# Performance work log

Measured on AMD Instinct MI355X. Metric: run time of the kernel, lower is better.

The kernel has to match this reference:

```python
import jax, jax.numpy as jnp
import numpy as np

B, S = 2, 1024
ENC_IN, MARK_IN = 21, 4
PRED_LEN, C_OUT = 96, 21
E = 512                 # embedding_dim
INNER = 2 * E           # proj_factor=2.0 (library default; Model does not pass it)
NH = 8                  # mLSTM heads
DH = INNER // NH        # 128
K = 4                   # causal conv1d kernel
BS = 4                  # qkv_proj_blocksize
NHP = INNER // BS       # 256 block-diagonal proj heads
NB = 4                  # num_blocks
EPS = 1e-5


def setup_inputs() -> dict:
    key = jax.random.key(0)
    ks = jax.random.split(key, 24)
    it = iter(range(24))
    def n(shape, s=0.02):
        return jax.random.normal(ks[next(it)], shape, jnp.float32) * s
    return {
        "x_enc": n((B, S, ENC_IN), 1.0),
        "x_mark_enc": n((B, S, MARK_IN), 1.0),
        "x_dec": n((B, PRED_LEN, ENC_IN), 1.0),
        "x_mark_dec": n((B, PRED_LEN, MARK_IN), 1.0),
        "emb_W": n((ENC_IN + MARK_IN, E), 0.05),
        "emb_b": jnp.zeros((E,), jnp.float32),
        "ln_w": jnp.ones((NB, E), jnp.float32),
        "up_W": n((NB, E, 2 * INNER)),
        "conv_W": n((NB, INNER, K), 0.1),
        "conv_b": jnp.zeros((NB, INNER), jnp.float32),
        "q_W": n((NB, NHP, BS, BS), 0.1),
        "k_W": n((NB, NHP, BS, BS), 0.1),
        "v_W": n((NB, NHP, BS, BS), 0.1),
        "ig_W": n((NB, 3 * INNER, NH)),
        "ig_b": jnp.zeros((NB, NH), jnp.float32),
        "fg_W": n((NB, 3 * INNER, NH)),
        "fg_b": jnp.tile(jnp.linspace(3.0, 6.0, NH, dtype=jnp.float32), (NB, 1)),
        "skip": jnp.ones((NB, INNER), jnp.float32),
        "onorm_w": jnp.ones((NB, INNER), jnp.float32),
        "down_W": n((NB, INNER, E)),
        "post_ln_w": jnp.ones((E,), jnp.float32),
        "head_W": n((E, C_OUT), 0.05),
        "head_b": jnp.zeros((C_OUT,), jnp.float32),
    }


def _ln(x, w):
    mu = jnp.mean(x, -1, keepdims=True)
    var = jnp.var(x, -1, keepdims=True)
    return (x - mu) * jax.lax.rsqrt(var + EPS) * w


def _headwise(x, w):
    # block-diagonal LinearHeadwiseExpand: (B,S,INNER) with (NHP,BS,BS) blocks
    xh = x.reshape(x.shape[0], x.shape[1], NHP, BS)
    return jnp.einsum('bshd,hod->bsho', xh, w).reshape(x.shape)


def _block(x, lw, uW, cW, cb, qW, kW, vW, igW, igb, fgW, fgb, sk, ow, dW):
    xn = _ln(x, lw)
    up = xn @ uW                                  # (B,S,2*INNER)
    xm, z = up[..., :INNER], up[..., INNER:]
    # causal depthwise conv1d + SiLU
    xc = jax.lax.conv_general_dilated(
        xm.transpose(0, 2, 1), cW[:, None, :], (1,), [(K - 1, 0)],
        feature_group_count=INNER,
        dimension_numbers=('NCH', 'OIH', 'NCH')).transpose(0, 2, 1) + cb
    xc = jax.nn.silu(xc)
    q = _headwise(xc, qW)
    k = _headwise(xc, kW)
    v = _headwise(xm, vW)
    qkv = jnp.concatenate([q, k, v], -1)          # (B,S,3*INNER)
    ig = (qkv @ igW + igb).transpose(0, 2, 1)     # (B,NH,S)
    fg = (qkv @ fgW + fgb).transpose(0, 2, 1)
    qh = q.reshape(B, S, NH, DH).transpose(0, 2, 1, 3)
    kh = k.reshape(B, S, NH, DH).transpose(0, 2, 1, 3)
    vh = v.reshape(B, S, NH, DH).transpose(0, 2, 1, 3)
    # parallel stabilized mLSTM (exp-gated linear attention)
    log_f = jax.nn.log_sigmoid(fg)
    cs = jnp.cumsum(log_f, -1)                    # (B,NH,S)
    Mmat = cs[..., :, None] - cs[..., None, :]    # (B,NH,S,S) cumulative decay
    tri = jnp.tril(jnp.ones((S, S), bool))
    logD = jnp.where(tri, Mmat + ig[..., None, :], -jnp.inf)
    m = jnp.max(logD, -1, keepdims=True)          # row-wise stabilizer
    D = jnp.exp(logD - m)
    qk = jnp.einsum('bnsd,bntd->bnst', qh, kh) / (DH ** 0.5)
    C = qk * D
    norm = jnp.maximum(jnp.abs(jnp.sum(C, -1, keepdims=True)), jnp.exp(-m))
    h = jnp.einsum('bnst,bntd->bnsd', C / (norm + 1e-6), vh)
    # multi-head layernorm (groupnorm over DH per head), weight, no bias
    hn = (h - jnp.mean(h, -1, keepdims=True)) * jax.lax.rsqrt(jnp.var(h, -1, keepdims=True) + EPS)
    hn = hn.transpose(0, 2, 1, 3).reshape(B, S, INNER) * ow
    hs = (hn + sk * xc) * jax.nn.silu(z)          # learnable skip + output gate
    return x + hs @ dW                            # residual


def reference(x_enc, x_mark_enc, x_dec, x_mark_dec, emb_W, emb_b, ln_w, up_W,
              conv_W, conv_b, q_W, k_W, v_W, ig_W, ig_b, fg_W, fg_b, skip,
              onorm_w, down_W, post_ln_w, head_W, head_b):
    x = jnp.concatenate([x_enc, x_mark_enc], -1) @ emb_W + emb_b
    for i in range(NB):
        x = _block(x, ln_w[i], up_W[i], conv_W[i], conv_b[i], q_W[i], k_W[i],
                   v_W[i], ig_W[i], ig_b[i], fg_W[i], fg_b[i], skip[i],
                   onorm_w[i], down_W[i])
    x = _ln(x, post_ln_w)
    return x[:, -PRED_LEN:, :] @ head_W + head_b
```

## Files before the change

### kernel.cpp

```cpp
#include <hip/hip_runtime.h>
#include <hip/hip_bf16.h>

#define S_LEN 1024
#define E_DIM 512
#define INNER_D 1024
#define NHEAD 8
#define DHEAD 128

typedef unsigned short u16;
typedef unsigned int u32;
typedef __attribute__((ext_vector_type(8))) short short8;
typedef __attribute__((ext_vector_type(4))) float f32x4;

union S8 { short8 v; u16 u[8]; uint4 q; };

__device__ __forceinline__ u16 f2bf(float f) {
  u32 u = __float_as_uint(f);
  u32 r = u + 0x7FFFu + ((u >> 16) & 1u);
  return (u16)(r >> 16);
}
__device__ __forceinline__ float bf2f(u16 u) { return __uint_as_float(((u32)u) << 16); }

__device__ __forceinline__ void gload16(const u16* g, u16* l) {
  __builtin_amdgcn_global_load_lds((const __attribute__((address_space(1))) void*)g,
                                   (__attribute__((address_space(3))) void*)l, 16, 0, 0);
}

__global__ __launch_bounds__(128) void embed_kernel(
    const float* __restrict__ xe, const float* __restrict__ xm,
    const float* __restrict__ W, const float* __restrict__ bias,
    float* __restrict__ x)
{
  int row = blockIdx.x;
  int tid = threadIdx.x;
  __shared__ float in_s[25];
  if (tid < 21) in_s[tid] = xe[row * 21 + tid];
  else if (tid < 25) in_s[tid] = xm[row * 4 + tid - 21];
  __syncthreads();
#pragma unroll
  for (int rep = 0; rep < 4; rep++) {
    int e = tid + rep * 128;
    float acc = bias[e];
#pragma unroll
    for (int i = 0; i < 25; i++) acc += in_s[i] * W[i * E_DIM + e];
    x[(size_t)row * E_DIM + e] = acc;
  }
}

__global__ __launch_bounds__(256) void ln_kernel(
    const float* __restrict__ x, const float* __restrict__ w, u16* __restrict__ out)
{
  int row = blockIdx.x, tid = threadIdx.x;
  const float* xr = x + (size_t)row * E_DIM;
  float2 v = *(const float2*)(xr + tid * 2);
  float s = v.x + v.y, q = v.x * v.x + v.y * v.y;
#pragma unroll
  for (int off = 32; off; off >>= 1) { s += __shfl_xor(s, off); q += __shfl_xor(q, off); }
  __shared__ float ssum[4], ssq[4];
  int wv = tid >> 6;
  if ((tid & 63) == 0) { ssum[wv] = s; ssq[wv] = q; }
  __syncthreads();
  s = ssum[0] + ssum[1] + ssum[2] + ssum[3];
  q = ssq[0] + ssq[1] + ssq[2] + ssq[3];
  float mu = s * (1.f / E_DIM);
  float var = q * (1.f / E_DIM) - mu * mu;
  float rs = rsqrtf(var + 1e-5f);
  int e = tid * 2;
  ushort2 o;
  o.x = f2bf((v.x - mu) * rs * w[e]);
  o.y = f2bf((v.y - mu) * rs * w[e + 1]);
  *(ushort2*)(out + (size_t)row * E_DIM + e) = o;
}

__global__ __launch_bounds__(256) void ln_final_kernel(
    const float* __restrict__ x, const float* __restrict__ w, float* __restrict__ out)
{
  int ridx = blockIdx.x;
  int b = ridx / 96, r = ridx % 96;
  int row = b * S_LEN + (S_LEN - 96) + r;
  int tid = threadIdx.x;
  const float* xr = x + (size_t)row * E_DIM;
  float2 v = *(const float2*)(xr + tid * 2);
  float s = v.x + v.y, q = v.x * v.x + v.y * v.y;
#pragma unroll
  for (int off = 32; off; off >>= 1) { s += __shfl_xor(s, off); q += __shfl_xor(q, off); }
  __shared__ float ssum[4], ssq[4];
  int wv = tid >> 6;
  if ((tid & 63) == 0) { ssum[wv] = s; ssq[wv] = q; }
  __syncthreads();
  s = ssum[0] + ssum[1] + ssum[2] + ssum[3];
  q = ssq[0] + ssq[1] + ssq[2] + ssq[3];
  float mu = s * (1.f / E_DIM);
  float var = q * (1.f / E_DIM) - mu * mu;
  float rs = rsqrtf(var + 1e-5f);
  int e = tid * 2;
  float2 o;
  o.x = (v.x - mu) * rs * w[e];
  o.y = (v.y - mu) * rs * w[e + 1];
  *(float2*)(out + (size_t)ridx * E_DIM + e) = o;
}

__global__ __launch_bounds__(256) void transpose_bf16_all_kernel(
    const float* __restrict__ in0, u16* __restrict__ out0, int K, int N)
{
  __shared__ u16 T[64][72];
  int L = blockIdx.z;
  const float* in = in0 + (size_t)L * K * N;
  u16* out = out0 + (size_t)L * N * K;
  int k0 = blockIdx.x * 64, n0 = blockIdx.y * 64;
  int t = threadIdx.x;
  int kr = t >> 2, nseg = (t & 3) * 16;
  const float* src = in + (size_t)(k0 + kr) * N + n0 + nseg;
#pragma unroll
  for (int j = 0; j < 16; j++) T[kr][nseg + j] = f2bf(src[j]);
  __syncthreads();
  int nr = t >> 2, kseg = (t & 3) * 16;
  u32 u[8];
#pragma unroll
  for (int rr = 0; rr < 8; rr++) {
    u32 lo = T[kseg + 2 * rr][nr];
    u32 hi = T[kseg + 2 * rr + 1][nr];
    u[rr] = lo | (hi << 16);
  }
  u16* dst = out + (size_t)(n0 + nr) * K + k0 + kseg;
  uint4 w0 = {u[0], u[1], u[2], u[3]};
  uint4 w1 = {u[4], u[5], u[6], u[7]};
  *(uint4*)dst = w0;
  *(uint4*)(dst + 8) = w1;
}

__global__ __launch_bounds__(256) void gates_w_transpose_kernel(
    const float* __restrict__ igW, const float* __restrict__ fgW,
    u16* __restrict__ hi, u16* __restrict__ lo)
{
  int L = blockIdx.z;
  int n = blockIdx.y;
  int k = blockIdx.x * 256 + threadIdx.x;
  const float* W = ((n < 8) ? igW : fgW) + (size_t)L * 24576;
  float v = W[(size_t)k * 8 + (n & 7)];
  u16 h = f2bf(v);
  u16 l = f2bf(v - bf2f(h));
  size_t o = ((size_t)L * 16 + n) * 3072 + k;
  hi[o] = h;
  lo[o] = l;
}

__global__ __launch_bounds__(256) void gemm_bf16_split64(
    const u16* __restrict__ A, const u16* __restrict__ Bt,
    float* __restrict__ C0, u16* __restrict__ C1,
    int M, int N, int K, int split_col, int ldc)
{
  __shared__ u16 As0[64 * 64], As1[64 * 64];
  __shared__ u16 Bs0[128 * 64], Bs1[128 * 64];
  const int tid = threadIdx.x;
  const int row0 = blockIdx.y * 64, col0 = blockIdx.x * 128;
  const int wave = tid >> 6, lane = tid & 63;
  const int wr = wave >> 1, wc = wave & 1;
  const int lm = lane & 15, lq = lane >> 4;
  const int lr = lane >> 3;
  const int cg = (lane & 7) ^ lr;
  f32x4 acc[2][4] = {};
  const u16* Abase = A + (size_t)(row0 + lr) * K + cg * 8;
  const u16* Bbase = Bt + (size_t)(col0 + lr) * K + cg * 8;
  const int key = lm & 7;

#define STAGE_UP(AS, BS, K0) do { \
  _Pragma("unroll") for (int i = 0; i < 2; i++) \
    gload16(Abase + (size_t)((wave * 2 + i) * 8) * K + (K0), &AS[(wave * 2 + i) * 512]); \
  _Pragma("unroll") for (int j = 0; j < 4; j++) \
    gload16(Bbase + (size_t)((wave * 4 + j) * 8) * K + (K0), &BS[(wave * 4 + j) * 512]); \
} while (0)

#define COMPUTE_UP(AS, BS) do { \
  short8 af[2][2], bfv[2][4]; \
  _Pragma("unroll") for (int kc = 0; kc < 2; kc++) { \
    _Pragma("unroll") for (int i = 0; i < 2; i++) \
      af[kc][i] = *(const short8*)&AS[(wr * 32 + i * 16 + lm) * 64 + (((kc * 4 + lq) ^ key) * 8)]; \
    _Pragma("unroll") for (int j = 0; j < 4; j++) \
      bfv[kc][j] = *(const short8*)&BS[(wc * 64 + j * 16 + lm) * 64 + (((kc * 4 + lq) ^ key) * 8)]; \
  } \
  _Pragma("unroll") for (int kc = 0; kc < 2; kc++) \
    _Pragma("unroll") for (int i = 0; i < 2; i++) \
      _Pragma("unroll") for (int j = 0; j < 4; j++) \
        acc[i][j] = __builtin_amdgcn_mfma_f32_16x16x32_bf16(af[kc][i], bfv[kc][j], acc[i][j], 0, 0, 0); \
} while (0)

  STAGE_UP(As0, Bs0, 0);
  STAGE_UP(As1, Bs1, 64);
#pragma unroll
  for (int t = 0; t < 8; t++) {
    if (t < 7) asm volatile("s_waitcnt vmcnt(6)" ::: "memory");
    else       asm volatile("s_waitcnt vmcnt(0)" ::: "memory");
    __builtin_amdgcn_sched_barrier(0);
    __builtin_amdgcn_s_barrier();
    if (t & 1) COMPUTE_UP(As1, Bs1); else COMPUTE_UP(As0, Bs0);
    __builtin_amdgcn_s_barrier();
    if (t + 2 < 8) {
      if (t & 1) STAGE_UP(As1, Bs1, (t + 2) * 64);
      else       STAGE_UP(As0, Bs0, (t + 2) * 64);
    }
  }
#undef STAGE_UP
#undef COMPUTE_UP

  const bool toC1 = (col0 >= split_col);
#pragma unroll
  for (int i = 0; i < 2; i++) {
#pragma unroll
    for (int j = 0; j < 4; j++) {
      int col = col0 - (toC1 ? split_col : 0) + wc * 64 + j * 16 + lm;
#pragma unroll
      for (int r = 0; r < 4; r++) {
        int row = row0 + wr * 32 + i * 16 + lq * 4 + r;
        if (toC1) C1[(size_t)row * ldc + col] = f2bf(acc[i][j][r]);
        else C0[(size_t)row * ldc + col] = acc[i][j][r];
      }
    }
  }
}

__global__ __launch_bounds__(256) void gemm_bf16_32(
    const u16* __restrict__ A, const u16* __restrict__ Bt,
    float* __restrict__ C, int M, int N, int K, int ldc)
{
  __shared__ u16 As0[64 * 64], As1[64 * 64];
  __shared__ u16 Bs0[64 * 64], Bs1[64 * 64];
  const int tid = threadIdx.x;
  const int row0 = blockIdx.y * 64, col0 = blockIdx.x * 64;
  const int wave = tid >> 6, lane = tid & 63;
  const int wr = wave >> 1, wc = wave & 1;
  const int lm = lane & 15, lq = lane >> 4;
  const int lr = lane >> 3;
  const int cg = (lane & 7) ^ lr;
  f32x4 acc[2][2] = {};
  const u16* Abase = A + (size_t)(row0 + lr) * K + cg * 8;
  const u16* Bbase = Bt + (size_t)(col0 + lr) * K + cg * 8;
  const int key = lm & 7;

#define STAGE_DN(AS, BS, K0) do { \
  _Pragma("unroll") for (int i = 0; i < 2; i++) \
    gload16(Abase + (size_t)((wave * 2 + i) * 8) * K + (K0), &AS[(wave * 2 + i) * 512]); \
  _Pragma("unroll") for (int j = 0; j < 2; j++) \
    gload16(Bbase + (size_t)((wave * 2 + j) * 8) * K + (K0), &BS[(wave * 2 + j) * 512]); \
} while (0)

#define COMPUTE_DN(AS, BS) do { \
  short8 af[2][2], bfv[2][2]; \
  _Pragma("unroll") for (int kc = 0; kc < 2; kc++) { \
    _Pragma("unroll") for (int i = 0; i < 2; i++) \
      af[kc][i] = *(const short8*)&AS[(wr * 32 + i * 16 + lm) * 64 + (((kc * 4 + lq) ^ key) * 8)]; \
    _Pragma("unroll") for (int j = 0; j < 2; j++) \
      bfv[kc][j] = *(const short8*)&BS[(wc * 32 + j * 16 + lm) * 64 + (((kc * 4 + lq) ^ key) * 8)]; \
  } \
  _Pragma("unroll") for (int kc = 0; kc < 2; kc++) \
    _Pragma("unroll") for (int i = 0; i < 2; i++) \
      _Pragma("unroll") for (int j = 0; j < 2; j++) \
        acc[i][j] = __builtin_amdgcn_mfma_f32_16x16x32_bf16(af[kc][i], bfv[kc][j], acc[i][j], 0, 0, 0); \
} while (0)

  STAGE_DN(As0, Bs0, 0);
  STAGE_DN(As1, Bs1, 64);
#pragma unroll
  for (int t = 0; t < 16; t++) {
    if (t < 15) asm volatile("s_waitcnt vmcnt(4)" ::: "memory");
    else        asm volatile("s_waitcnt vmcnt(0)" ::: "memory");
    __builtin_amdgcn_sched_barrier(0);
    __builtin_amdgcn_s_barrier();
    if (t & 1) COMPUTE_DN(As1, Bs1); else COMPUTE_DN(As0, Bs0);
    __builtin_amdgcn_s_barrier();
    if (t + 2 < 16) {
      if (t & 1) STAGE_DN(As1, Bs1, (t + 2) * 64);
      else       STAGE_DN(As0, Bs0, (t + 2) * 64);
    }
  }
#undef STAGE_DN
#undef COMPUTE_DN

#pragma unroll
  for (int i = 0; i < 2; i++) {
#pragma unroll
    for (int j = 0; j < 2; j++) {
      int col = col0 + wc * 32 + j * 16 + lm;
#pragma unroll
      for (int r = 0; r < 4; r++) {
        int row = row0 + wr * 32 + i * 16 + lq * 4 + r;
        C[(size_t)row * ldc + col] += acc[i][j][r];
      }
    }
  }
}

__global__ __launch_bounds__(256) void convqkv_kernel(
    const float* __restrict__ xm,
    const float* __restrict__ cw, const float* __restrict__ cb,
    const float* __restrict__ qw, const float* __restrict__ kw, const float* __restrict__ vw,
    float* __restrict__ xc, u16* __restrict__ q, u16* __restrict__ k, u16* __restrict__ v)
{
  int r0 = blockIdx.x * 4;
  int s0 = r0 & (S_LEN - 1);
  int g = threadIdx.x;
  int c0 = g * 4;
  const float* base = xm + (size_t)r0 * INNER_D + c0;

  float4 xv[7];
#pragma unroll
  for (int j = 0; j < 7; j++) {
    int ts = s0 - 3 + j;
    float4 t = {0.f, 0.f, 0.f, 0.f};
    if (ts >= 0) t = *(const float4*)(base + (ptrdiff_t)(j - 3) * INNER_D);
    xv[j] = t;
  }
  float cwv[4][4];
#pragma unroll
  for (int c = 0; c < 4; c++)
#pragma unroll
    for (int kk = 0; kk < 4; kk++) cwv[c][kk] = cw[(c0 + c) * 4 + kk];
  float cbv[4] = {cb[c0], cb[c0 + 1], cb[c0 + 2], cb[c0 + 3]};
  const float* qg = qw + g * 16;
  const float* kg = kw + g * 16;
  const float* vg = vw + g * 16;
  float qwv[16], kwv[16], vwv[16];
#pragma unroll
  for (int i = 0; i < 16; i++) { qwv[i] = qg[i]; kwv[i] = kg[i]; vwv[i] = vg[i]; }

#pragma unroll
  for (int i = 0; i < 4; i++) {
    float a0 = cbv[0], a1 = cbv[1], a2 = cbv[2], a3 = cbv[3];
#pragma unroll
    for (int kk = 0; kk < 4; kk++) {
      float4 xvv = xv[i + kk];
      a0 += xvv.x * cwv[0][kk];
      a1 += xvv.y * cwv[1][kk];
      a2 += xvv.z * cwv[2][kk];
      a3 += xvv.w * cwv[3][kk];
    }
    a0 = a0 / (1.f + __expf(-a0));
    a1 = a1 / (1.f + __expf(-a1));
    a2 = a2 / (1.f + __expf(-a2));
    a3 = a3 / (1.f + __expf(-a3));
    float4 accv = {a0, a1, a2, a3};
    *(float4*)(xc + (size_t)(r0 + i) * INNER_D + c0) = accv;

    float xcv[4] = {a0, a1, a2, a3};
    float xmv[4] = {xv[i + 3].x, xv[i + 3].y, xv[i + 3].z, xv[i + 3].w};
    ushort4 qs, ks, vs;
    u16* qp = (u16*)&qs; u16* kp = (u16*)&ks; u16* vp = (u16*)&vs;
#pragma unroll
    for (int o = 0; o < 4; o++) {
      float aq = 0.f, ak = 0.f, av = 0.f;
#pragma unroll
      for (int d = 0; d < 4; d++) {
        aq += xcv[d] * qwv[o * 4 + d];
        ak += xcv[d] * kwv[o * 4 + d];
        av += xmv[d] * vwv[o * 4 + d];
      }
      qp[o] = f2bf(aq); kp[o] = f2bf(ak); vp[o] = f2bf(av);
    }
    size_t off = (size_t)(r0 + i) * INNER_D + c0;
    *(ushort4*)(q + off) = qs;
    *(ushort4*)(k + off) = ks;
    *(ushort4*)(v + off) = vs;
  }
}

__global__ __launch_bounds__(256) void gates_mfma_kernel(
    const u16* __restrict__ q, const u16* __restrict__ k, const u16* __restrict__ v,
    const u16* __restrict__ whi, const u16* __restrict__ wlo,
    const float* __restrict__ igb, const float* __restrict__ fgb,
    float* __restrict__ ig, float* __restrict__ fg)
{
  const int blk = blockIdx.x;
  const int tid = threadIdx.x;
  const int wave = tid >> 6, lane = tid & 63;
  const int lm = lane & 15, lq = lane >> 4;
  const int grow = blk * 16 + lm;
  const u16* parts[3] = {q, k, v};
  f32x4 acc = {};
#pragma unroll 4
  for (int kc = 0; kc < 24; kc++) {
    int k0 = wave * 768 + kc * 32;
    int part = k0 >> 10;
    int idx = (k0 & 1023) + lq * 8;
    S8 a, bh_, bl_;
    a.q = *(const uint4*)(parts[part] + (size_t)grow * INNER_D + idx);
    bh_.q = *(const uint4*)(whi + (size_t)lm * 3072 + k0 + lq * 8);
    bl_.q = *(const uint4*)(wlo + (size_t)lm * 3072 + k0 + lq * 8);
    acc = __builtin_amdgcn_mfma_f32_16x16x32_bf16(a.v, bh_.v, acc, 0, 0, 0);
    acc = __builtin_amdgcn_mfma_f32_16x16x32_bf16(a.v, bl_.v, acc, 0, 0, 0);
  }
  __shared__ float red[4][16][17];
#pragma unroll
  for (int r = 0; r < 4; r++) red[wave][lq * 4 + r][lm] = acc[r];
  __syncthreads();
  if (wave == 0) {
#pragma unroll
    for (int r = 0; r < 4; r++) {
      int row = lq * 4 + r;
      float sum = red[0][row][lm] + red[1][row][lm] + red[2][row][lm] + red[3][row][lm];
      int growr = blk * 16 + row;
      int b = growr >> 10, s = growr & (S_LEN - 1);
      if (lm < 8) ig[((size_t)(b * NHEAD + lm) << 10) + s] = sum + igb[lm];
      else        fg[((size_t)(b * NHEAD + (lm - 8)) << 10) + s] = sum + fgb[lm - 8];
    }
  }
}

__global__ __launch_bounds__(1024) void scan_kernel(
    const float* __restrict__ ig, const float* __restrict__ fg,
    float* __restrict__ a, float* __restrict__ rm, float* __restrict__ enm)
{
  int bh = blockIdx.x;
  int t = threadIdx.x;
  int lane = t & 63, wv = t >> 6;
  __shared__ float sw[16];
  size_t o = ((size_t)bh << 10) + t;
  float f = fg[o];
  float lf = (f >= 0.f) ? -log1pf(__expf(-f)) : f - log1pf(__expf(f));
  float v = lf;
#pragma unroll
  for (int off = 1; off < 64; off <<= 1) {
    float u = __shfl_up(v, off);
    if (lane >= off) v += u;
  }
  if (lane == 63) sw[wv] = v;
  __syncthreads();
  float pre = 0.f;
  for (int w = 0; w < wv; w++) pre += sw[w];
  float cs = v + pre;
  float av = ig[o] - cs;
  a[o] = av;
  float m = av;
#pragma unroll
  for (int off = 1; off < 64; off <<= 1) {
    float u = __shfl_up(m, off);
    if (lane >= off) m = fmaxf(m, u);
  }
  __syncthreads();
  if (lane == 63) sw[wv] = m;
  __syncthreads();
  float pm = -3.4e38f;
  for (int w = 0; w < wv; w++) pm = fmaxf(pm, sw[w]);
  float rmx = fmaxf(m, pm);
  rm[o] = rmx;
  enm[o] = __expf(-(cs + rmx));
}

__device__ __constant__ int c_qt[24] = {7,15,14,15, 6,13,14,12,13, 5,11,12,10,11, 4, 9,10, 8, 9, 3, 8, 2, 1, 0};
__device__ __constant__ int c_k0[24] = {0, 0, 7, 8, 0, 0, 0, 6, 7, 0, 0, 0, 5, 6, 0, 0, 0, 4, 5, 0, 0, 0, 0, 0};
__device__ __constant__ int c_k1[24] = {8, 8,15,16, 7, 7, 7,13,14, 6, 6, 6,11,12, 5, 5, 5, 9,10, 4, 4, 3, 2, 1};
__device__ __constant__ int c_md[24] = {0, 1, 2, 2, 0, 1, 1, 2, 2, 0, 1, 1, 2, 2, 0, 1, 1, 2, 2, 0, 1, 0, 0, 0};

__global__ __launch_bounds__(256) void attn_mfma_kernel(
    const u16* __restrict__ qhg, const u16* __restrict__ khg, const u16* __restrict__ vhg,
    const float* __restrict__ a_arr, const float* __restrict__ rm_arr, const float* __restrict__ enm_arr,
    const float* __restrict__ xc, const u16* __restrict__ zh,
    const float* __restrict__ skip, const float* __restrict__ onw,
    u16* __restrict__ hs, float* __restrict__ hpart, float* __restrict__ scpart)
{
  const int bh = blockIdx.x;
  const int job = blockIdx.y;
  const int qt = c_qt[job], k0t = c_k0[job], k1t = c_k1[job], mode = c_md[job];
  const int b = bh >> 3, h = bh & 7;
  const int s0 = qt * 64;
  const int tid = threadIdx.x;
  const int wave = tid >> 6, lane = tid & 63;
  const int lm = lane & 15, lq = lane >> 4;
  const size_t rowbase = (size_t)b * S_LEN;
  const int c0 = h * DHEAD;

  __shared__ u16 Ks0[64 * 128], Ks1[64 * 128];
  __shared__ u16 Vt0[128 * 72], Vt1[128 * 72];
  __shared__ u16 Ws[64 * 72];
  __shared__ float as0[64], as1[64];

  short8 aq[4];
  {
    const u16* qp = qhg + (rowbase + s0 + wave * 16 + lm) * INNER_D + c0 + lq * 8;
#pragma unroll
    for (int kc = 0; kc < 4; kc++) {
      S8 tmp; tmp.q = *(const uint4*)(qp + kc * 32);
      aq[kc] = tmp.v;
    }
  }
  float rmv[4];
#pragma unroll
  for (int r = 0; r < 4; r++)
    rmv[r] = rm_arr[(size_t)bh * S_LEN + s0 + wave * 16 + lq * 4 + r];

  f32x4 accH[8] = {};
  float sc_acc[4] = {0.f, 0.f, 0.f, 0.f};
  const float scale = 0.08838834764831845f;
  const int lr16 = lane >> 4;
  const int ls16 = lane & 15;
  const int tp0 = tid & 31, dg0 = tid >> 5;
  const int dg1 = dg0 + 8;

  S8 vA0, vA1, vB0, vB1;
  float aval;

#define PREF_K(KS, T0) do { \
  _Pragma("unroll") for (int j = 0; j < 4; j++) { \
    int rK = (wave * 4 + j) * 4 + lr16; \
    int cgk = ls16 ^ (rK & 7); \
    gload16(khg + (rowbase + (T0) + rK) * INNER_D + c0 + cgk * 8, &KS[(wave * 4 + j) * 512]); \
  } \
} while (0)

#define PREF_V(T0) do { \
  const u16* sv = vhg + (rowbase + (T0) + 2 * tp0) * INNER_D + c0 + dg0 * 8; \
  vA0.q = *(const uint4*)sv; \
  vA1.q = *(const uint4*)(sv + INNER_D); \
  const u16* sw2 = vhg + (rowbase + (T0) + 2 * tp0) * INNER_D + c0 + dg1 * 8; \
  vB0.q = *(const uint4*)sw2; \
  vB1.q = *(const uint4*)(sw2 + INNER_D); \
  aval = (tid < 64) ? a_arr[(size_t)bh * S_LEN + (T0) + tid] : 0.f; \
} while (0)

#define WRITE_V(VT, ASB) do { \
  _Pragma("unroll") for (int j = 0; j < 8; j++) \
    *(u32*)&VT[(dg0 * 8 + j) * 72 + 2 * tp0] = (u32)vA0.u[j] | ((u32)vA1.u[j] << 16); \
  _Pragma("unroll") for (int j = 0; j < 8; j++) \
    *(u32*)&VT[(dg1 * 8 + j) * 72 + 2 * tp0] = (u32)vB0.u[j] | ((u32)vB1.u[j] << 16); \
  if (tid < 64) ASB[tid] = aval; \
} while (0)

#define QK_STEP(KS, PACC) do { \
  _Pragma("unroll") for (int kc = 0; kc < 4; kc++) \
    _Pragma("unroll") for (int cb = 0; cb < 4; cb++) { \
      short8 bk = *(const short8*)&KS[(cb * 16 + lm) * 128 + (((kc * 4 + lq) ^ (lm & 7)) * 8)]; \
      PACC[cb] = __builtin_amdgcn_mfma_f32_16x16x32_bf16(aq[kc], bk, PACC[cb], 0, 0, 0); \
    } \
} while (0)

#define W_PV(ASB, VT, T0, PACC) do { \
  float wpart[4] = {0.f, 0.f, 0.f, 0.f}; \
  _Pragma("unroll") for (int cb = 0; cb < 4; cb++) { \
    int colg = (T0) + cb * 16 + lm; \
    float ea = ASB[cb * 16 + lm]; \
    _Pragma("unroll") for (int r = 0; r < 4; r++) { \
      int rowg = s0 + wave * 16 + lq * 4 + r; \
      float wv = PACC[cb][r] * scale * __expf(ea - rmv[r]); \
      if (colg > rowg) wv = 0.f; \
      wpart[r] += wv; \
      Ws[(wave * 16 + lq * 4 + r) * 72 + cb * 16 + lm] = f2bf(wv); \
    } \
  } \
  _Pragma("unroll") for (int r = 0; r < 4; r++) { \
    float sr = wpart[r]; \
    sr += __shfl_xor(sr, 1); sr += __shfl_xor(sr, 2); \
    sr += __shfl_xor(sr, 4); sr += __shfl_xor(sr, 8); \
    sc_acc[r] += sr; \
  } \
  _Pragma("unroll") for (int kc = 0; kc < 2; kc++) { \
    short8 aw = *(const short8*)&Ws[(wave * 16 + lm) * 72 + kc * 32 + lq * 8]; \
    _Pragma("unroll") for (int nb = 0; nb < 8; nb++) { \
      short8 bv = *(const short8*)&VT[(nb * 16 + lm) * 72 + kc * 32 + lq * 8]; \
      accH[nb] = __builtin_amdgcn_mfma_f32_16x16x32_bf16(aw, bv, accH[nb], 0, 0, 0); \
    } \
  } \
} while (0)

  int kt = k0t;
  PREF_K(Ks0, kt * 64);
  PREF_V(kt * 64);
  WRITE_V(Vt0, as0);
  __syncthreads();

  while (true) {
    {
      bool more = (kt + 1 < k1t);
      if (more) { PREF_K(Ks1, (kt + 1) * 64); PREF_V((kt + 1) * 64); }
      f32x4 pacc[4] = {};
      QK_STEP(Ks0, pacc);
      if (more) WRITE_V(Vt1, as1);
      W_PV(as0, Vt0, kt * 64, pacc);
      __syncthreads();
      kt++;
      if (kt >= k1t) break;
    }
    {
      bool more = (kt + 1 < k1t);
      if (more) { PREF_K(Ks0, (kt + 1) * 64); PREF_V((kt + 1) * 64); }
      f32x4 pacc[4] = {};
      QK_STEP(Ks1, pacc);
      if (more) WRITE_V(Vt0, as0);
      W_PV(as1, Vt1, kt * 64, pacc);
      __syncthreads();
      kt++;
      if (kt >= k1t) break;
    }
  }
#undef PREF_K
#undef PREF_V
#undef WRITE_V
#undef QK_STEP
#undef W_PV

  if (mode != 0) {
    int slot = mode - 1;
    int qr = qt - 8;
    float* Hp = hpart + (((size_t)slot * 16 + bh) * 8 + qr) * 8192;
    float* sp = scpart + ((slot * 16 + bh) * 8 + qr) * 64;
#pragma unroll
    for (int r = 0; r < 4; r++) {
      int row = wave * 16 + lq * 4 + r;
      if (lm == 0) sp[row] = sc_acc[r];
#pragma unroll
      for (int nb = 0; nb < 8; nb++)
        Hp[row * 128 + nb * 16 + lm] = accH[nb][r];
    }
    return;
  }

  float inv[4], muv[4], rsv[4];
#pragma unroll
  for (int r = 0; r < 4; r++) {
    int rowg = s0 + wave * 16 + lq * 4 + r;
    float nrm = fmaxf(fabsf(sc_acc[r]), enm_arr[(size_t)bh * S_LEN + rowg]);
    inv[r] = 1.f / (nrm + 1e-6f);
  }
#pragma unroll
  for (int r = 0; r < 4; r++) {
    float s = 0.f, qq = 0.f;
#pragma unroll
    for (int nb = 0; nb < 8; nb++) {
      float hv = accH[nb][r] * inv[r];
      accH[nb][r] = hv;
      s += hv; qq += hv * hv;
    }
    s += __shfl_xor(s, 1); s += __shfl_xor(s, 2); s += __shfl_xor(s, 4); s += __shfl_xor(s, 8);
    qq += __shfl_xor(qq, 1); qq += __shfl_xor(qq, 2); qq += __shfl_xor(qq, 4); qq += __shfl_xor(qq, 8);
    float mu = s * (1.f / DHEAD);
    float var = qq * (1.f / DHEAD) - mu * mu;
    muv[r] = mu;
    rsv[r] = rsqrtf(var + 1e-5f);
  }
  float ow[8], sk[8];
#pragma unroll
  for (int nb = 0; nb < 8; nb++) {
    ow[nb] = onw[c0 + nb * 16 + lm];
    sk[nb] = skip[c0 + nb * 16 + lm];
  }
#pragma unroll
  for (int r = 0; r < 4; r++) {
    int rowg = s0 + wave * 16 + lq * 4 + r;
    size_t base = (rowbase + rowg) * INNER_D + c0;
#pragma unroll
    for (int nb = 0; nb < 8; nb++) {
      int d = nb * 16 + lm;
      float xcv = xc[base + d];
      float zv = bf2f(zh[base + d]);
      float hn = (accH[nb][r] - muv[r]) * rsv[r] * ow[nb] + sk[nb] * xcv;
      float o = hn * (zv / (1.f + __expf(-zv)));
      hs[base + d] = f2bf(o);
    }
  }
}

__global__ __launch_bounds__(256) void attn_combine_kernel(
    const float* __restrict__ hpart, const float* __restrict__ scpart,
    const float* __restrict__ enm,
    const float* __restrict__ xc, const u16* __restrict__ zh,
    const float* __restrict__ skip, const float* __restrict__ onw,
    u16* __restrict__ hs)
{
  int wave = threadIdx.x >> 6, lane = threadIdx.x & 63;
  int gid = blockIdx.x * 4 + wave;
  int bh = gid >> 9;
  int rr = gid & 511;
  int qr = rr >> 6, row = rr & 63;
  int b = bh >> 3, hh = bh & 7;
  int s = (qr + 8) * 64 + row;
  size_t off = (((size_t)bh) * 8 + qr) * 8192 + row * 128 + lane * 2;
  float2 h0 = *(const float2*)(hpart + off);
  float2 h1 = *(const float2*)(hpart + 1048576 + off);
  int sidx = (bh * 8 + qr) * 64 + row;
  float sc = scpart[sidx] + scpart[8192 + sidx];
  float nrm = fmaxf(fabsf(sc), enm[(size_t)bh * S_LEN + s]);
  float inv = 1.f / (nrm + 1e-6f);
  float hx = (h0.x + h1.x) * inv, hy = (h0.y + h1.y) * inv;
  float sm = hx + hy, sq = hx * hx + hy * hy;
#pragma unroll
  for (int off2 = 32; off2; off2 >>= 1) { sm += __shfl_xor(sm, off2); sq += __shfl_xor(sq, off2); }
  float mu = sm * (1.f / DHEAD);
  float var = sq * (1.f / DHEAD) - mu * mu;
  float rs = rsqrtf(var + 1e-5f);
  int c0 = hh * DHEAD + lane * 2;
  size_t base = ((size_t)(b * S_LEN + s)) * INNER_D + c0;
  float2 xc2 = *(const float2*)(xc + base);
  ushort2 z2u = *(const ushort2*)(zh + base);
  float z2x = bf2f(z2u.x), z2y = bf2f(z2u.y);
  float skx = skip[c0], sky = skip[c0 + 1];
  float owx = onw[c0],  owy = onw[c0 + 1];
  ushort2 o;
  o.x = f2bf(((hx - mu) * rs * owx + skx * xc2.x) * (z2x / (1.f + __expf(-z2x))));
  o.y = f2bf(((hy - mu) * rs * owy + sky * xc2.y) * (z2y / (1.f + __expf(-z2y))));
  *(ushort2*)(hs + base) = o;
}

__global__ __launch_bounds__(64) void head_kernel(
    const float* __restrict__ ln96, const float* __restrict__ hW, const float* __restrict__ hb,
    float* __restrict__ out)
{
  int row = blockIdx.x;
  int n = threadIdx.x;
  if (n >= 21) return;
  float acc = hb[n];
  const float* xr = ln96 + (size_t)row * E_DIM;
  for (int kk = 0; kk < E_DIM; kk++) acc += xr[kk] * hW[kk * 21 + n];
  out[row * 21 + n] = acc;
}

extern "C" void kernel_launch(void* const* d_in, const int* in_sizes, int n_in,
                              void* d_out, int out_size, void* d_ws, size_t ws_size,
                              hipStream_t stream)
{
  const float* x_enc   = (const float*)d_in[0];
  const float* x_mark  = (const float*)d_in[1];
  const float* emb_W   = (const float*)d_in[4];
  const float* emb_b   = (const float*)d_in[5];
  const float* ln_w    = (const float*)d_in[6];
  const float* up_W    = (const float*)d_in[7];
  const float* conv_W  = (const float*)d_in[8];
  const float* conv_b  = (const float*)d_in[9];
  const float* q_W     = (const float*)d_in[10];
  const float* k_W     = (const float*)d_in[11];
  const float* v_W     = (const float*)d_in[12];
  const float* ig_W    = (const float*)d_in[13];
  const float* ig_b    = (const float*)d_in[14];
  const float* fg_W    = (const float*)d_in[15];
  const float* fg_b    = (const float*)d_in[16];
  const float* skip_w  = (const float*)d_in[17];
  const float* onorm_w = (const float*)d_in[18];
  const float* down_W  = (const float*)d_in[19];
  const float* post_ln = (const float*)d_in[20];
  const float* head_W  = (const float*)d_in[21];
  const float* head_b  = (const float*)d_in[22];

  float* p = (float*)d_ws;
  float* x    = p; p += 1048576;
  float* xm   = p; p += 2097152;
  float* xc   = p; p += 2097152;
  float* igb_ = p; p += 16384;
  float* fgb_ = p; p += 16384;
  float* ab   = p; p += 16384;
  float* rmb  = p; p += 16384;
  float* enmb = p; p += 16384;
  float* ln96 = p; p += 98304;
  u16* qhb = (u16*)p; p += 1048576;
  u16* khb = (u16*)p; p += 1048576;
  u16* vhb = (u16*)p; p += 1048576;
  u16* zh  = (u16*)p; p += 524288;
  u16* xnh = (u16*)p; p += 524288;
  u16* upWtA = (u16*)p; p += 2097152;
  u16* dnWtA = (u16*)p; p += 1048576;
  u16* gtwH = (u16*)p; p += 98304;
  u16* gtwL = (u16*)p; p += 98304;
  float* hpart = p; p += 2097152;
  float* scpart = p; p += 16384;
  u16* hsbh = (u16*)xm;

  embed_kernel<<<2048, 128, 0, stream>>>(x_enc, x_mark, emb_W, emb_b, x);
  transpose_bf16_all_kernel<<<dim3(8, 32, 4), 256, 0, stream>>>(up_W, upWtA, 512, 2048);
  transpose_bf16_all_kernel<<<dim3(16, 8, 4), 256, 0, stream>>>(down_W, dnWtA, 1024, 512);
  gates_w_transpose_kernel<<<dim3(12, 16, 4), 256, 0, stream>>>(ig_W, fg_W, gtwH, gtwL);

  for (int L = 0; L < 4; L++) {
    ln_kernel<<<2048, 256, 0, stream>>>(x, ln_w + L * 512, xnh);
    gemm_bf16_split64<<<dim3(16, 32), 256, 0, stream>>>(
        xnh, upWtA + (size_t)L * 1048576, xm, zh, 2048, 2048, 512, 1024, 1024);
    convqkv_kernel<<<512, 256, 0, stream>>>(
        xm, conv_W + L * 4096, conv_b + L * 1024,
        q_W + L * 4096, k_W + L * 4096, v_W + L * 4096,
        xc, qhb, khb, vhb);
    gates_mfma_kernel<<<128, 256, 0, stream>>>(
        qhb, khb, vhb, gtwH + (size_t)L * 49152, gtwL + (size_t)L * 49152,
        ig_b + L * 8, fg_b + L * 8, igb_, fgb_);
    scan_kernel<<<16, 1024, 0, stream>>>(igb_, fgb_, ab, rmb, enmb);
    attn_mfma_kernel<<<dim3(16, 24), 256, 0, stream>>>(
        qhb, khb, vhb, ab, rmb, enmb, xc, zh,
        skip_w + L * 1024, onorm_w + L * 1024, hsbh, hpart, scpart);
    attn_combine_kernel<<<2048, 256, 0, stream>>>(
        hpart, scpart, enmb, xc, zh, skip_w + L * 1024, onorm_w + L * 1024, hsbh);
    gemm_bf16_32<<<dim3(8, 32), 256, 0, stream>>>(
        hsbh, dnWtA + (size_t)L * 524288, x, 2048, 512, 1024, 512);
  }

  ln_final_kernel<<<192, 256, 0, stream>>>(x, post_ln, ln96);
  head_kernel<<<192, 64, 0, stream>>>(ln96, head_W, head_b, (float*)d_out);
}
```

Baseline: 494.2 us.

## Fuse final layernorm with head, widen conv rows per block, add MFMA priority hints

Merges the final layernorm and output-head projection into one kernel. The head dot products are split across 8 slices and reduced in shared memory, which drops a launch and the intermediate buffer round trip. Each convqkv block now processes 8 rows instead of 4, so the overlapping conv halo is loaded less often, at the cost of half as many blocks. s_setprio hints are placed around MFMA sections in the gates and attention kernels to favour matrix-issue waves.

```diff
diff --git a/kernel.cpp b/kernel.cpp
--- a/kernel.cpp
+++ b/kernel.cpp
@@ -72,8 +72,10 @@
   *(ushort2*)(out + (size_t)row * E_DIM + e) = o;
 }
 
-__global__ __launch_bounds__(256) void ln_final_kernel(
-    const float* __restrict__ x, const float* __restrict__ w, float* __restrict__ out)
+__global__ __launch_bounds__(256) void lnhead_kernel(
+    const float* __restrict__ x, const float* __restrict__ w,
+    const float* __restrict__ hW, const float* __restrict__ hb,
+    float* __restrict__ out)
 {
   int ridx = blockIdx.x;
   int b = ridx / 96, r = ridx % 96;
@@ -85,6 +87,8 @@
 #pragma unroll
   for (int off = 32; off; off >>= 1) { s += __shfl_xor(s, off); q += __shfl_xor(q, off); }
   __shared__ float ssum[4], ssq[4];
+  __shared__ float lnv[512];
+  __shared__ float part[8][32];
   int wv = tid >> 6;
   if ((tid & 63) == 0) { ssum[wv] = s; ssq[wv] = q; }
   __syncthreads();
@@ -94,10 +98,24 @@
   float var = q * (1.f / E_DIM) - mu * mu;
   float rs = rsqrtf(var + 1e-5f);
   int e = tid * 2;
-  float2 o;
-  o.x = (v.x - mu) * rs * w[e];
-  o.y = (v.y - mu) * rs * w[e + 1];
-  *(float2*)(out + (size_t)ridx * E_DIM + e) = o;
+  lnv[e]     = (v.x - mu) * rs * w[e];
+  lnv[e + 1] = (v.y - mu) * rs * w[e + 1];
+  __syncthreads();
+  int n = tid & 31, sl = tid >> 5;
+  float p = 0.f;
+  if (n < 21) {
+#pragma unroll 8
+    for (int kk = 0; kk < 64; kk++)
+      p += lnv[sl * 64 + kk] * hW[(sl * 64 + kk) * 21 + n];
+  }
+  part[sl][n] = p;
+  __syncthreads();
+  if (tid < 21) {
+    float acc = hb[tid];
+#pragma unroll
+    for (int j = 0; j < 8; j++) acc += part[j][tid];
+    out[ridx * 21 + tid] = acc;
+  }
 }
 
 __global__ __launch_bounds__(256) void transpose_bf16_all_kernel(
@@ -296,15 +314,15 @@
     const float* __restrict__ qw, const float* __restrict__ kw, const float* __restrict__ vw,
     float* __restrict__ xc, u16* __restrict__ q, u16* __restrict__ k, u16* __restrict__ v)
 {
-  int r0 = blockIdx.x * 4;
+  int r0 = blockIdx.x * 8;
   int s0 = r0 & (S_LEN - 1);
   int g = threadIdx.x;
   int c0 = g * 4;
   const float* base = xm + (size_t)r0 * INNER_D + c0;
 
-  float4 xv[7];
-#pragma unroll
-  for (int j = 0; j < 7; j++) {
+  float4 xv[11];
+#pragma unroll
+  for (int j = 0; j < 11; j++) {
     int ts = s0 - 3 + j;
     float4 t = {0.f, 0.f, 0.f, 0.f};
     if (ts >= 0) t = *(const float4*)(base + (ptrdiff_t)(j - 3) * INNER_D);
@@ -324,7 +342,7 @@
   for (int i = 0; i < 16; i++) { qwv[i] = qg[i]; kwv[i] = kg[i]; vwv[i] = vg[i]; }
 
 #pragma unroll
-  for (int i = 0; i < 4; i++) {
+  for (int i = 0; i < 8; i++) {
     float a0 = cbv[0], a1 = cbv[1], a2 = cbv[2], a3 = cbv[3];
 #pragma unroll
     for (int kk = 0; kk < 4; kk++) {
@@ -385,8 +403,10 @@
     a.q = *(const uint4*)(parts[part] + (size_t)grow * INNER_D + idx);
     bh_.q = *(const uint4*)(whi + (size_t)lm * 3072 + k0 + lq * 8);
     bl_.q = *(const uint4*)(wlo + (size_t)lm * 3072 + k0 + lq * 8);
+    __builtin_amdgcn_s_setprio(1);
     acc = __builtin_amdgcn_mfma_f32_16x16x32_bf16(a.v, bh_.v, acc, 0, 0, 0);
     acc = __builtin_amdgcn_mfma_f32_16x16x32_bf16(a.v, bl_.v, acc, 0, 0, 0);
+    __builtin_amdgcn_s_setprio(0);
   }
   __shared__ float red[4][16][17];
 #pragma unroll
@@ -525,11 +545,13 @@
 } while (0)
 
 #define QK_STEP(KS, PACC) do { \
+  __builtin_amdgcn_s_setprio(1); \
   _Pragma("unroll") for (int kc = 0; kc < 4; kc++) \
     _Pragma("unroll") for (int cb = 0; cb < 4; cb++) { \
       short8 bk = *(const short8*)&KS[(cb * 16 + lm) * 128 + (((kc * 4 + lq) ^ (lm & 7)) * 8)]; \
       PACC[cb] = __builtin_amdgcn_mfma_f32_16x16x32_bf16(aq[kc], bk, PACC[cb], 0, 0, 0); \
     } \
+  __builtin_amdgcn_s_setprio(0); \
 } while (0)
 
 #define W_PV(ASB, VT, T0, PACC) do { \
@@ -551,6 +573,7 @@
     sr += __shfl_xor(sr, 4); sr += __shfl_xor(sr, 8); \
     sc_acc[r] += sr; \
   } \
+  __builtin_amdgcn_s_setprio(1); \
   _Pragma("unroll") for (int kc = 0; kc < 2; kc++) { \
     short8 aw = *(const short8*)&Ws[(wave * 16 + lm) * 72 + kc * 32 + lq * 8]; \
     _Pragma("unroll") for (int nb = 0; nb < 8; nb++) { \
@@ -558,6 +581,7 @@
       accH[nb] = __builtin_amdgcn_mfma_f32_16x16x32_bf16(aw, bv, accH[nb], 0, 0, 0); \
     } \
   } \
+  __builtin_amdgcn_s_setprio(0); \
 } while (0)
 
   int kt = k0t;
@@ -696,19 +720,6 @@
   o.x = f2bf(((hx - mu) * rs * owx + skx * xc2.x) * (z2x / (1.f + __expf(-z2x))));
   o.y = f2bf(((hy - mu) * rs * owy + sky * xc2.y) * (z2y / (1.f + __expf(-z2y))));
   *(ushort2*)(hs + base) = o;
-}
-
-__global__ __launch_bounds__(64) void head_kernel(
-    const float* __restrict__ ln96, const float* __restrict__ hW, const float* __restrict__ hb,
-    float* __restrict__ out)
-{
-  int row = blockIdx.x;
-  int n = threadIdx.x;
-  if (n >= 21) return;
-  float acc = hb[n];
-  const float* xr = ln96 + (size_t)row * E_DIM;
-  for (int kk = 0; kk < E_DIM; kk++) acc += xr[kk] * hW[kk * 21 + n];
-  out[row * 21 + n] = acc;
 }
 
 extern "C" void kernel_launch(void* const* d_in, const int* in_sizes, int n_in,
@@ -769,7 +780,7 @@
     ln_kernel<<<2048, 256, 0, stream>>>(x, ln_w + L * 512, xnh);
     gemm_bf16_split64<<<dim3(16, 32), 256, 0, stream>>>(
         xnh, upWtA + (size_t)L * 1048576, xm, zh, 2048, 2048, 512, 1024, 1024);
-    convqkv_kernel<<<512, 256, 0, stream>>>(
+    convqkv_kernel<<<256, 256, 0, stream>>>(
         xm, conv_W + L * 4096, conv_b + L * 1024,
         q_W + L * 4096, k_W + L * 4096, v_W + L * 4096,
         xc, qhb, khb, vhb);
@@ -786,6 +797,5 @@
         hsbh, dnWtA + (size_t)L * 524288, x, 2048, 512, 1024, 512);
   }
 
-  ln_final_kernel<<<192, 256, 0, stream>>>(x, post_ln, ln96);
-  head_kernel<<<192, 64, 0, stream>>>(ln96, head_W, head_b, (float*)d_out);
-}
+  lnhead_kernel<<<192, 256, 0, stream>>>(x, post_ln, head_W, head_b, (float*)d_out);
+}
```

Result: faster. 472.1 us (-4.5%).
